# Kernel tuning notes

Hardware: AMD Instinct MI355X
Metric: run time of the kernel (lower is better)

The kernel has to match this reference:

```python
import jax, jax.numpy as jnp
import numpy as np

IN_DIM = 256
OUT_DIM = 256


def setup_inputs() -> dict:
    key = jax.random.key(0)
    k1, k2, k3, k4 = jax.random.split(key, 4)
    B, N = 8, 2048
    X = jax.random.normal(k1, (B, N, IN_DIM), dtype=jnp.float32)
    adj = jax.random.uniform(k2, (B, N, N), dtype=jnp.float32)
    # nn.Linear(input_dim, output_dim): W is [out, in], bias [out]
    bound = 1.0 / np.sqrt(IN_DIM)
    W = jax.random.uniform(k3, (OUT_DIM, IN_DIM), minval=-bound, maxval=bound, dtype=jnp.float32)
    b = jax.random.uniform(k4, (OUT_DIM,), minval=-bound, maxval=bound, dtype=jnp.float32)
    return {"X": X, "adj": adj, "W": W, "b": b}


def reference(X, adj, W, b):
    N = adj.shape[-1]
    # adj_hat = adj + I
    adj_hat = adj + jnp.eye(N, dtype=adj.dtype)
    # D^{-1/2} A_hat D^{-1/2}: diag matmuls are just row/col scaling
    d = jnp.sum(adj_hat, axis=-1) ** -0.5  # [B, N]
    adj_norm = d[..., :, None] * adj_hat * d[..., None, :]
    # aggregate then linear + relu
    H = jnp.matmul(adj_norm, X)  # [B, N, F_in]
    out = jnp.einsum('bnf,of->bno', H, W) + b
    return jax.nn.relu(out)
```

## Files before the change

kernel.cpp:

```cpp
#include <hip/hip_runtime.h>
#include <stdint.h>

typedef __attribute__((ext_vector_type(8))) short bf16x8;
typedef __attribute__((ext_vector_type(4))) float f32x4;
typedef unsigned short u16;

constexpr int NN = 2048, NF = 256;

__device__ inline u16 f2bf(float f) {
  uint32_t u = __builtin_bit_cast(uint32_t, f);
  uint32_t r = (u + 0x7FFFu + ((u >> 16) & 1u)) >> 16;
  return (u16)r;
}
__device__ inline float bf2f(u16 h) {
  uint32_t u = ((uint32_t)h) << 16;
  return __builtin_bit_cast(float, u);
}

__device__ inline void gload_lds16(const void* g, void* l) {
  __builtin_amdgcn_global_load_lds(
      (const __attribute__((address_space(1))) uint32_t*)g,
      (__attribute__((address_space(3))) uint32_t*)l,
      16, 0, 0);
}

__global__ __launch_bounds__(256) void k_rowsum(const float* __restrict__ adj,
                                                u16* __restrict__ adjb,
                                                float* __restrict__ d,
                                                const float* __restrict__ W,
                                                u16* __restrict__ Wb) {
  if (blockIdx.x >= 16384) {
    int i = (blockIdx.x - 16384) * 256 + threadIdx.x;
    float4 v = ((const float4*)W)[i];
    ushort4 o;
    o.x = f2bf(v.x); o.y = f2bf(v.y); o.z = f2bf(v.z); o.w = f2bf(v.w);
    *(ushort4*)(Wb + (size_t)i * 4) = o;
    return;
  }
  int row = blockIdx.x;
  const float4* p = (const float4*)(adj + (size_t)row * NN);
  u16* ob = adjb + (size_t)row * NN;
  float s = 0.f;
#pragma unroll
  for (int c = 0; c < 2; ++c) {
    int idx = threadIdx.x + 256 * c;
    float4 v = p[idx];
    s += v.x + v.y + v.z + v.w;
    ushort4 o;
    o.x = f2bf(v.x); o.y = f2bf(v.y); o.z = f2bf(v.z); o.w = f2bf(v.w);
    *(ushort4*)(ob + (size_t)idx * 4) = o;
  }
#pragma unroll
  for (int off = 32; off > 0; off >>= 1) s += __shfl_down(s, off, 64);
  __shared__ float red[4];
  int lane = threadIdx.x & 63, w = threadIdx.x >> 6;
  if (lane == 0) red[w] = s;
  __syncthreads();
  if (threadIdx.x == 0) {
    float t = red[0] + red[1] + red[2] + red[3] + 1.0f;
    d[row] = 1.0f / sqrtf(t);
  }
}

__global__ __launch_bounds__(256) void k_xprep(const float* __restrict__ X,
                                               const float* __restrict__ d,
                                               u16* __restrict__ XpT) {
  int jt = blockIdx.x, ft = blockIdx.y, b = blockIdx.z;
  int j0 = jt * 64, f0 = ft * 64;
  __shared__ u16 T[64][66];
  int t = threadIdx.x;
#pragma unroll
  for (int s = 0; s < 4; ++s) {
    int q = s * 256 + t;
    int r = q >> 4, c4 = q & 15;
    int j = j0 + r;
    float dv = d[b * NN + j];
    float4 v = *(const float4*)(X + ((size_t)(b * NN + j)) * NF + f0 + c4 * 4);
    T[r][c4 * 4 + 0] = f2bf(v.x * dv);
    T[r][c4 * 4 + 1] = f2bf(v.y * dv);
    T[r][c4 * 4 + 2] = f2bf(v.z * dv);
    T[r][c4 * 4 + 3] = f2bf(v.w * dv);
  }
  __syncthreads();
#pragma unroll
  for (int s = 0; s < 4; ++s) {
    int q = s * 256 + t;
    int fr = q >> 4, c4 = q & 15;
    int f = f0 + fr;
    int swz = (f >> 1) & 3;
    int joff = (c4 * 4) ^ (swz << 3);
    ushort4 o;
    o.x = T[c4 * 4 + 0][fr]; o.y = T[c4 * 4 + 1][fr];
    o.z = T[c4 * 4 + 2][fr]; o.w = T[c4 * 4 + 3][fr];
    *(ushort4*)(XpT + ((size_t)(b * NF + f)) * NN + j0 + joff) = o;
  }
}

__global__ __launch_bounds__(256, 2) void k_fused(
    const u16* __restrict__ adjb, const u16* __restrict__ XpT,
    const float* __restrict__ dsc, const u16* __restrict__ Wb,
    const float* __restrict__ bias, float* __restrict__ out) {
  int flat = blockIdx.x;
  int b = flat & 7, mt = flat >> 3;
  int i0 = mt * 32;

  __shared__ __align__(16) char smem[36864];
  u16* Hs = (u16*)smem;

  int t = threadIdx.x;
  int lane = t & 63, w = t >> 6;
  int l15 = lane & 15, l4 = lane >> 4;
  int wc = w;

  const u16* adjbb = adjb + ((size_t)b * NN + i0) * NN;
  const u16* XpTb = XpT + (size_t)b * NF * NN;

  int rl = (w << 3) + ((lane & 31) >> 2);
  int asrc_off = ((lane & 3) ^ ((rl >> 1) & 3)) * 8;
  const u16* a_src = adjbb + (size_t)rl * NN + asrc_off;

  f32x4 acc[2][4] = {};

  if (lane < 32) gload_lds16(a_src, smem + (w << 9));
#pragma unroll
  for (int c = 0; c < 4; ++c) {
    int q = c * 256 + t;
    gload_lds16(XpTb + (size_t)(q >> 2) * NN + (q & 3) * 8,
                smem + 4096 + (size_t)(c * 256 + w * 64) * 16);
  }
  __syncthreads();

  for (int k = 0; k < 64; ++k) {
    char* Ac = smem + ((k & 1) << 11);
    char* An = smem + (((k & 1) ^ 1) << 11);
    char* Bc = smem + 4096 + ((k & 1) << 14);
    char* Bn = smem + 4096 + (((k & 1) ^ 1) << 14);

    bf16x8 af[2], bfr[4];
#pragma unroll
    for (int mi = 0; mi < 2; ++mi) {
      int r = mi * 16 + l15;
      af[mi] = *(const bf16x8*)(Ac + r * 64 + ((l4 ^ ((r >> 1) & 3)) << 4));
    }
#pragma unroll
    for (int ni = 0; ni < 4; ++ni) {
      int n = wc * 64 + ni * 16 + l15;
      bfr[ni] = *(const bf16x8*)(Bc + n * 64 + ((l4 ^ ((n >> 1) & 3)) << 4));
    }
    __builtin_amdgcn_sched_barrier(0);

    if (k < 63) {
      int k2 = (k + 1) * 32;
      if (lane < 32) gload_lds16(a_src + k2, An + (w << 9));
#pragma unroll
      for (int c = 0; c < 4; ++c) {
        int q = c * 256 + t;
        gload_lds16(XpTb + (size_t)(q >> 2) * NN + k2 + (q & 3) * 8,
                    Bn + (size_t)(c * 256 + w * 64) * 16);
      }
    }
    __builtin_amdgcn_sched_barrier(0);

    __builtin_amdgcn_s_setprio(1);
#pragma unroll
    for (int mi = 0; mi < 2; ++mi)
#pragma unroll
      for (int ni = 0; ni < 4; ++ni)
        acc[mi][ni] = __builtin_amdgcn_mfma_f32_16x16x32_bf16(af[mi], bfr[ni],
                                                              acc[mi][ni], 0, 0, 0);
    __builtin_amdgcn_s_setprio(0);
    __builtin_amdgcn_sched_barrier(0);
    __syncthreads();
  }

  const float* db = dsc + b * NN;
#pragma unroll
  for (int mi = 0; mi < 2; ++mi) {
#pragma unroll
    for (int ni = 0; ni < 4; ++ni) {
      int f = wc * 64 + ni * 16 + l15;
      int swz8 = ((f >> 1) & 3) << 3;
      ushort4 xv = *(const ushort4*)(XpTb + (size_t)f * NN + i0 +
                                     ((mi * 16 + l4 * 4) ^ swz8));
#pragma unroll
      for (int qq = 0; qq < 4; ++qq) {
        int il = mi * 16 + l4 * 4 + qq;
        float dv = db[i0 + il];
        float xpv = bf2f(((const u16*)&xv)[qq]);
        float hv = dv * (acc[mi][ni][qq] + xpv);
        Hs[il * 264 + f] = f2bf(hv);
      }
    }
  }
  __syncthreads();

  f32x4 acc2[2][4] = {};
#pragma unroll
  for (int kk = 0; kk < 256; kk += 32) {
    bf16x8 a2[2], b2[4];
#pragma unroll
    for (int mi = 0; mi < 2; ++mi) {
      int r = mi * 16 + l15;
      a2[mi] = *(const bf16x8*)&Hs[r * 264 + kk + l4 * 8];
    }
#pragma unroll
    for (int ni = 0; ni < 4; ++ni) {
      int o = wc * 64 + ni * 16 + l15;
      b2[ni] = *(const bf16x8*)&Wb[(size_t)o * 256 + kk + l4 * 8];
    }
#pragma unroll
    for (int mi = 0; mi < 2; ++mi)
#pragma unroll
      for (int ni = 0; ni < 4; ++ni)
        acc2[mi][ni] = __builtin_amdgcn_mfma_f32_16x16x32_bf16(a2[mi], b2[ni],
                                                               acc2[mi][ni], 0, 0, 0);
  }

  float* outb = out + ((size_t)b * NN + i0) * NF;
#pragma unroll
  for (int mi = 0; mi < 2; ++mi) {
#pragma unroll
    for (int qq = 0; qq < 4; ++qq) {
      int il = mi * 16 + l4 * 4 + qq;
#pragma unroll
      for (int ni = 0; ni < 4; ++ni) {
        int o = wc * 64 + ni * 16 + l15;
        float v = acc2[mi][ni][qq] + bias[o];
        outb[(size_t)il * NF + o] = fmaxf(v, 0.f);
      }
    }
  }
}

extern "C" void kernel_launch(void* const* d_in, const int* in_sizes, int n_in,
                              void* d_out, int out_size, void* d_ws, size_t ws_size,
                              hipStream_t stream) {
  const float* X    = (const float*)d_in[0];
  const float* adj  = (const float*)d_in[1];
  const float* W    = (const float*)d_in[2];
  const float* bias = (const float*)d_in[3];
  float* out = (float*)d_out;

  char* ws = (char*)d_ws;
  float* dsc  = (float*)(ws);
  u16*   Wb   = (u16*)(ws + 65536);
  u16*   XpT  = (u16*)(ws + 262144);
  u16*   adjb = (u16*)(ws + 262144 + 8388608);

  k_rowsum<<<dim3(16448), dim3(256), 0, stream>>>(adj, adjb, dsc, W, Wb);
  k_xprep<<<dim3(32, 4, 8), dim3(256), 0, stream>>>(X, dsc, XpT);
  k_fused<<<dim3(512), dim3(256), 0, stream>>>(adjb, XpT, dsc, Wb, bias, out);
}
```

Measured before the change: 85.73 us.

## Load B operand directly from global into registers, drop LDS staging for XpT

The main K loop now loads each wave's XpT fragments straight from global memory into registers, double-buffered two steps ahead. Only the adjacency tile goes through LDS, as a 4-deep ring with explicit vmcnt waits and barriers. The XpT swizzle is removed since it no longer feeds LDS, and LDS use drops so more blocks can fit per CU. This trades LDS traffic and space for uncoalesced-ish 16-byte global reads per lane and hand-tuned waitcnt accounting that must be exactly right.

```diff
diff --git a/kernel.cpp b/kernel.cpp
--- a/kernel.cpp
+++ b/kernel.cpp
@@ -86,15 +86,48 @@
   for (int s = 0; s < 4; ++s) {
     int q = s * 256 + t;
     int fr = q >> 4, c4 = q & 15;
-    int f = f0 + fr;
-    int swz = (f >> 1) & 3;
-    int joff = (c4 * 4) ^ (swz << 3);
     ushort4 o;
     o.x = T[c4 * 4 + 0][fr]; o.y = T[c4 * 4 + 1][fr];
     o.z = T[c4 * 4 + 2][fr]; o.w = T[c4 * 4 + 3][fr];
-    *(ushort4*)(XpT + ((size_t)(b * NF + f)) * NN + j0 + joff) = o;
-  }
-}
+    *(ushort4*)(XpT + ((size_t)(b * NF + f0 + fr)) * NN + j0 + c4 * 4) = o;
+  }
+}
+
+#define FUSED_STEP(K, BR, VMC, DO_ISSUE)                                       \
+  {                                                                            \
+    asm volatile("s_waitcnt vmcnt(" VMC ")" ::: "memory");                     \
+    __builtin_amdgcn_sched_barrier(0);                                         \
+    __builtin_amdgcn_s_barrier();                                              \
+    if (DO_ISSUE) {                                                            \
+      if (lane < 32)                                                           \
+        gload_lds16(a_src + (size_t)((K) + 2) * 32,                            \
+                    smem + ((((K) + 2) & 3) << 11) + (w << 9));                \
+    }                                                                          \
+    __builtin_amdgcn_sched_barrier(0);                                         \
+    char* Ab = smem + (((K) & 3) << 11);                                       \
+    bf16x8 af0 = *(const bf16x8*)(Ab + aoff0);                                 \
+    bf16x8 af1 = *(const bf16x8*)(Ab + aoff1);                                 \
+    asm volatile("s_waitcnt lgkmcnt(0)" ::: "memory");                         \
+    __builtin_amdgcn_sched_barrier(0);                                         \
+    __builtin_amdgcn_s_setprio(1);                                             \
+    acc[0][0] = __builtin_amdgcn_mfma_f32_16x16x32_bf16(af0, BR[0], acc[0][0], 0, 0, 0); \
+    acc[0][1] = __builtin_amdgcn_mfma_f32_16x16x32_bf16(af0, BR[1], acc[0][1], 0, 0, 0); \
+    acc[0][2] = __builtin_amdgcn_mfma_f32_16x16x32_bf16(af0, BR[2], acc[0][2], 0, 0, 0); \
+    acc[0][3] = __builtin_amdgcn_mfma_f32_16x16x32_bf16(af0, BR[3], acc[0][3], 0, 0, 0); \
+    acc[1][0] = __builtin_amdgcn_mfma_f32_16x16x32_bf16(af1, BR[0], acc[1][0], 0, 0, 0); \
+    acc[1][1] = __builtin_amdgcn_mfma_f32_16x16x32_bf16(af1, BR[1], acc[1][1], 0, 0, 0); \
+    acc[1][2] = __builtin_amdgcn_mfma_f32_16x16x32_bf16(af1, BR[2], acc[1][2], 0, 0, 0); \
+    acc[1][3] = __builtin_amdgcn_mfma_f32_16x16x32_bf16(af1, BR[3], acc[1][3], 0, 0, 0); \
+    __builtin_amdgcn_s_setprio(0);                                             \
+    __builtin_amdgcn_sched_barrier(0);                                         \
+    if (DO_ISSUE) {                                                            \
+      BR[0] = *(const bf16x8*)(bp0 + (size_t)((K) + 2) * 32);                  \
+      BR[1] = *(const bf16x8*)(bp1 + (size_t)((K) + 2) * 32);                  \
+      BR[2] = *(const bf16x8*)(bp2 + (size_t)((K) + 2) * 32);                  \
+      BR[3] = *(const bf16x8*)(bp3 + (size_t)((K) + 2) * 32);                  \
+    }                                                                          \
+    __builtin_amdgcn_sched_barrier(0);                                         \
+  }
 
 __global__ __launch_bounds__(256, 2) void k_fused(
     const u16* __restrict__ adjb, const u16* __restrict__ XpT,
@@ -104,7 +137,7 @@
   int b = flat & 7, mt = flat >> 3;
   int i0 = mt * 32;
 
-  __shared__ __align__(16) char smem[36864];
+  __shared__ __align__(16) char smem[17408];
   u16* Hs = (u16*)smem;
 
   int t = threadIdx.x;
@@ -119,59 +152,40 @@
   int asrc_off = ((lane & 3) ^ ((rl >> 1) & 3)) * 8;
   const u16* a_src = adjbb + (size_t)rl * NN + asrc_off;
 
+  int aoff0 = l15 * 64 + ((l4 ^ ((l15 >> 1) & 3)) << 4);
+  int aoff1 = aoff0 + 1024;
+
+  const u16* bp0 = XpTb + (size_t)(wc * 64 + l15) * NN + l4 * 8;
+  const u16* bp1 = bp0 + (size_t)16 * NN;
+  const u16* bp2 = bp0 + (size_t)32 * NN;
+  const u16* bp3 = bp0 + (size_t)48 * NN;
+
   f32x4 acc[2][4] = {};
+  bf16x8 brA[4], brB[4];
 
   if (lane < 32) gload_lds16(a_src, smem + (w << 9));
-#pragma unroll
-  for (int c = 0; c < 4; ++c) {
-    int q = c * 256 + t;
-    gload_lds16(XpTb + (size_t)(q >> 2) * NN + (q & 3) * 8,
-                smem + 4096 + (size_t)(c * 256 + w * 64) * 16);
-  }
-  __syncthreads();
-
-  for (int k = 0; k < 64; ++k) {
-    char* Ac = smem + ((k & 1) << 11);
-    char* An = smem + (((k & 1) ^ 1) << 11);
-    char* Bc = smem + 4096 + ((k & 1) << 14);
-    char* Bn = smem + 4096 + (((k & 1) ^ 1) << 14);
-
-    bf16x8 af[2], bfr[4];
-#pragma unroll
-    for (int mi = 0; mi < 2; ++mi) {
-      int r = mi * 16 + l15;
-      af[mi] = *(const bf16x8*)(Ac + r * 64 + ((l4 ^ ((r >> 1) & 3)) << 4));
-    }
-#pragma unroll
-    for (int ni = 0; ni < 4; ++ni) {
-      int n = wc * 64 + ni * 16 + l15;
-      bfr[ni] = *(const bf16x8*)(Bc + n * 64 + ((l4 ^ ((n >> 1) & 3)) << 4));
-    }
-    __builtin_amdgcn_sched_barrier(0);
-
-    if (k < 63) {
-      int k2 = (k + 1) * 32;
-      if (lane < 32) gload_lds16(a_src + k2, An + (w << 9));
-#pragma unroll
-      for (int c = 0; c < 4; ++c) {
-        int q = c * 256 + t;
-        gload_lds16(XpTb + (size_t)(q >> 2) * NN + k2 + (q & 3) * 8,
-                    Bn + (size_t)(c * 256 + w * 64) * 16);
-      }
-    }
-    __builtin_amdgcn_sched_barrier(0);
-
-    __builtin_amdgcn_s_setprio(1);
-#pragma unroll
-    for (int mi = 0; mi < 2; ++mi)
-#pragma unroll
-      for (int ni = 0; ni < 4; ++ni)
-        acc[mi][ni] = __builtin_amdgcn_mfma_f32_16x16x32_bf16(af[mi], bfr[ni],
-                                                              acc[mi][ni], 0, 0, 0);
-    __builtin_amdgcn_s_setprio(0);
-    __builtin_amdgcn_sched_barrier(0);
-    __syncthreads();
-  }
+  __builtin_amdgcn_sched_barrier(0);
+  brA[0] = *(const bf16x8*)(bp0);
+  brA[1] = *(const bf16x8*)(bp1);
+  brA[2] = *(const bf16x8*)(bp2);
+  brA[3] = *(const bf16x8*)(bp3);
+  __builtin_amdgcn_sched_barrier(0);
+  if (lane < 32) gload_lds16(a_src + 32, smem + 2048 + (w << 9));
+  __builtin_amdgcn_sched_barrier(0);
+  brB[0] = *(const bf16x8*)(bp0 + 32);
+  brB[1] = *(const bf16x8*)(bp1 + 32);
+  brB[2] = *(const bf16x8*)(bp2 + 32);
+  brB[3] = *(const bf16x8*)(bp3 + 32);
+  __builtin_amdgcn_sched_barrier(0);
+
+  for (int k2 = 0; k2 < 62; k2 += 2) {
+    FUSED_STEP(k2, brA, "9", true);
+    FUSED_STEP(k2 + 1, brB, "9", true);
+  }
+  FUSED_STEP(62, brA, "9", false);
+  FUSED_STEP(63, brB, "4", false);
+
+  __syncthreads();
 
   const float* db = dsc + b * NN;
 #pragma unroll
@@ -179,9 +193,7 @@
 #pragma unroll
     for (int ni = 0; ni < 4; ++ni) {
       int f = wc * 64 + ni * 16 + l15;
-      int swz8 = ((f >> 1) & 3) << 3;
-      ushort4 xv = *(const ushort4*)(XpTb + (size_t)f * NN + i0 +
-                                     ((mi * 16 + l4 * 4) ^ swz8));
+      ushort4 xv = *(const ushort4*)(XpTb + (size_t)f * NN + i0 + mi * 16 + l4 * 4);
 #pragma unroll
       for (int qq = 0; qq < 4; ++qq) {
         int il = mi * 16 + l4 * 4 + qq;
```

Result: slower. 113.0 us (+31.8%).

## Deepen k_fused main loop into multi-stage LDS pipeline with explicit vmcnt waits

Applied to the files above, without the earlier changes.

Replaces the double-buffered K loop in the fused aggregation kernel with a hand-unrolled pipeline. It uses three A buffers, each loaded as 64-wide chunks by all 256 threads every other step, and four B buffers with a prefetch distance of two steps. Explicit s_waitcnt vmcnt counts and bare s_barrier calls replace the full __syncthreads, so more global loads stay in flight. LDS use rises from 36 KB to 76 KB per block, which may reduce the number of resident blocks per CU, and correctness now depends on the hand-chosen wait counts and buffer rotation.

```diff
diff --git a/kernel.cpp b/kernel.cpp
--- a/kernel.cpp
+++ b/kernel.cpp
@@ -96,6 +96,50 @@
   }
 }
 
+#define BBASE 12288
+
+#define FUSED_STEP(K, AW, AR, BW, BRI, VMC, IA, IB)                            \
+  {                                                                            \
+    if (IA) {                                                                  \
+      gload_lds16(a_src + (size_t)((K) + 2) * 32,                              \
+                  smem + ((AW) << 12) + (w << 10));                            \
+    }                                                                          \
+    if (IB) {                                                                  \
+      _Pragma("unroll")                                                        \
+      for (int c = 0; c < 4; ++c) {                                            \
+        int q = c * 256 + t;                                                   \
+        gload_lds16(XpTb + (size_t)(q >> 2) * NN + ((K) + 2) * 32 + (q & 3) * 8, \
+                    smem + BBASE + ((BW) << 14) + (c * 256 + w * 64) * 16);    \
+      }                                                                        \
+    }                                                                          \
+    __builtin_amdgcn_sched_barrier(0);                                         \
+    asm volatile("s_waitcnt vmcnt(" VMC ")" ::: "memory");                     \
+    __builtin_amdgcn_sched_barrier(0);                                         \
+    __builtin_amdgcn_s_barrier();                                              \
+    __builtin_amdgcn_sched_barrier(0);                                         \
+    const char* Ab = smem + ((AR) << 12) + (((K) & 1) << 11);                  \
+    const char* Bb = smem + BBASE + ((BRI) << 14);                             \
+    bf16x8 af0 = *(const bf16x8*)(Ab + aoff0);                                 \
+    bf16x8 af1 = *(const bf16x8*)(Ab + aoff0 + 1024);                          \
+    bf16x8 b0 = *(const bf16x8*)(Bb + boff0);                                  \
+    bf16x8 b1 = *(const bf16x8*)(Bb + boff0 + 1024);                           \
+    bf16x8 b2 = *(const bf16x8*)(Bb + boff0 + 2048);                           \
+    bf16x8 b3 = *(const bf16x8*)(Bb + boff0 + 3072);                           \
+    asm volatile("s_waitcnt lgkmcnt(0)" ::: "memory");                         \
+    __builtin_amdgcn_sched_barrier(0);                                         \
+    __builtin_amdgcn_s_setprio(1);                                             \
+    acc[0][0] = __builtin_amdgcn_mfma_f32_16x16x32_bf16(af0, b0, acc[0][0], 0, 0, 0); \
+    acc[0][1] = __builtin_amdgcn_mfma_f32_16x16x32_bf16(af0, b1, acc[0][1], 0, 0, 0); \
+    acc[0][2] = __builtin_amdgcn_mfma_f32_16x16x32_bf16(af0, b2, acc[0][2], 0, 0, 0); \
+    acc[0][3] = __builtin_amdgcn_mfma_f32_16x16x32_bf16(af0, b3, acc[0][3], 0, 0, 0); \
+    acc[1][0] = __builtin_amdgcn_mfma_f32_16x16x32_bf16(af1, b0, acc[1][0], 0, 0, 0); \
+    acc[1][1] = __builtin_amdgcn_mfma_f32_16x16x32_bf16(af1, b1, acc[1][1], 0, 0, 0); \
+    acc[1][2] = __builtin_amdgcn_mfma_f32_16x16x32_bf16(af1, b2, acc[1][2], 0, 0, 0); \
+    acc[1][3] = __builtin_amdgcn_mfma_f32_16x16x32_bf16(af1, b3, acc[1][3], 0, 0, 0); \
+    __builtin_amdgcn_s_setprio(0);                                             \
+    __builtin_amdgcn_sched_barrier(0);                                         \
+  }
+
 __global__ __launch_bounds__(256, 2) void k_fused(
     const u16* __restrict__ adjb, const u16* __restrict__ XpT,
     const float* __restrict__ dsc, const u16* __restrict__ Wb,
@@ -104,7 +148,7 @@
   int b = flat & 7, mt = flat >> 3;
   int i0 = mt * 32;
 
-  __shared__ __align__(16) char smem[36864];
+  __shared__ __align__(16) char smem[77824];
   u16* Hs = (u16*)smem;
 
   int t = threadIdx.x;
@@ -115,63 +159,51 @@
   const u16* adjbb = adjb + ((size_t)b * NN + i0) * NN;
   const u16* XpTb = XpT + (size_t)b * NF * NN;
 
-  int rl = (w << 3) + ((lane & 31) >> 2);
-  int asrc_off = ((lane & 3) ^ ((rl >> 1) & 3)) * 8;
-  const u16* a_src = adjbb + (size_t)rl * NN + asrc_off;
+  int as_ = t >> 7, ar_ = (t >> 2) & 31, ac_ = t & 3;
+  const u16* a_src = adjbb + (size_t)ar_ * NN + as_ * 32 +
+                     ((ac_ ^ ((ar_ >> 1) & 3)) << 3);
+
+  int aoff0 = l15 * 64 + ((l4 ^ ((l15 >> 1) & 3)) << 4);
+  int n0 = wc * 64 + l15;
+  int boff0 = n0 * 64 + ((l4 ^ ((n0 >> 1) & 3)) << 4);
 
   f32x4 acc[2][4] = {};
 
-  if (lane < 32) gload_lds16(a_src, smem + (w << 9));
+  gload_lds16(a_src, smem + (w << 10));
 #pragma unroll
   for (int c = 0; c < 4; ++c) {
     int q = c * 256 + t;
     gload_lds16(XpTb + (size_t)(q >> 2) * NN + (q & 3) * 8,
-                smem + 4096 + (size_t)(c * 256 + w * 64) * 16);
-  }
-  __syncthreads();
-
-  for (int k = 0; k < 64; ++k) {
-    char* Ac = smem + ((k & 1) << 11);
-    char* An = smem + (((k & 1) ^ 1) << 11);
-    char* Bc = smem + 4096 + ((k & 1) << 14);
-    char* Bn = smem + 4096 + (((k & 1) ^ 1) << 14);
-
-    bf16x8 af[2], bfr[4];
-#pragma unroll
-    for (int mi = 0; mi < 2; ++mi) {
-      int r = mi * 16 + l15;
-      af[mi] = *(const bf16x8*)(Ac + r * 64 + ((l4 ^ ((r >> 1) & 3)) << 4));
-    }
-#pragma unroll
-    for (int ni = 0; ni < 4; ++ni) {
-      int n = wc * 64 + ni * 16 + l15;
-      bfr[ni] = *(const bf16x8*)(Bc + n * 64 + ((l4 ^ ((n >> 1) & 3)) << 4));
-    }
-    __builtin_amdgcn_sched_barrier(0);
-
-    if (k < 63) {
-      int k2 = (k + 1) * 32;
-      if (lane < 32) gload_lds16(a_src + k2, An + (w << 9));
-#pragma unroll
-      for (int c = 0; c < 4; ++c) {
-        int q = c * 256 + t;
-        gload_lds16(XpTb + (size_t)(q >> 2) * NN + k2 + (q & 3) * 8,
-                    Bn + (size_t)(c * 256 + w * 64) * 16);
-      }
-    }
-    __builtin_amdgcn_sched_barrier(0);
-
-    __builtin_amdgcn_s_setprio(1);
-#pragma unroll
-    for (int mi = 0; mi < 2; ++mi)
-#pragma unroll
-      for (int ni = 0; ni < 4; ++ni)
-        acc[mi][ni] = __builtin_amdgcn_mfma_f32_16x16x32_bf16(af[mi], bfr[ni],
-                                                              acc[mi][ni], 0, 0, 0);
-    __builtin_amdgcn_s_setprio(0);
-    __builtin_amdgcn_sched_barrier(0);
-    __syncthreads();
-  }
+                smem + BBASE + (c * 256 + w * 64) * 16);
+  }
+#pragma unroll
+  for (int c = 0; c < 4; ++c) {
+    int q = c * 256 + t;
+    gload_lds16(XpTb + (size_t)(q >> 2) * NN + 32 + (q & 3) * 8,
+                smem + BBASE + 16384 + (c * 256 + w * 64) * 16);
+  }
+  __builtin_amdgcn_sched_barrier(0);
+
+  for (int kb = 0; kb < 60; kb += 12) {
+    FUSED_STEP(kb + 0, 1, 0, 2, 0, "9", 1, 1)
+    FUSED_STEP(kb + 1, 0, 0, 3, 1, "9", 0, 1)
+    FUSED_STEP(kb + 2, 2, 1, 0, 2, "9", 1, 1)
+    FUSED_STEP(kb + 3, 0, 1, 1, 3, "9", 0, 1)
+    FUSED_STEP(kb + 4, 0, 2, 2, 0, "9", 1, 1)
+    FUSED_STEP(kb + 5, 0, 2, 3, 1, "9", 0, 1)
+    FUSED_STEP(kb + 6, 1, 0, 0, 2, "9", 1, 1)
+    FUSED_STEP(kb + 7, 0, 0, 1, 3, "9", 0, 1)
+    FUSED_STEP(kb + 8, 2, 1, 2, 0, "9", 1, 1)
+    FUSED_STEP(kb + 9, 0, 1, 3, 1, "9", 0, 1)
+    FUSED_STEP(kb + 10, 0, 2, 0, 2, "9", 1, 1)
+    FUSED_STEP(kb + 11, 0, 2, 1, 3, "9", 0, 1)
+  }
+  FUSED_STEP(60, 1, 0, 2, 0, "9", 1, 1)
+  FUSED_STEP(61, 0, 0, 3, 1, "9", 0, 1)
+  FUSED_STEP(62, 0, 1, 0, 2, "4", 0, 0)
+  FUSED_STEP(63, 0, 1, 0, 3, "0", 0, 0)
+
+  __syncthreads();
 
   const float* db = dsc + b * NN;
 #pragma unroll
```

Result: no change. 85.12 us (-0.7%).
